# Performance work log

Measured on AMD Instinct MI355X. Metric: run time of the kernel, lower is better.

## Reference

```python
import jax, jax.numpy as jnp
import numpy as np

LSTM_SIZE = 512
MEM_SIZE = 2048
MEM_DIM = 256
NB_READS = 4
GAMMA = 0.95
EPS = 1e-8
B = 64
IN_RAW = 256
IN_TOTAL = IN_RAW + NB_READS * MEM_SIZE  # 8448
PARAM_DIM = (2 * MEM_DIM + 1) * NB_READS  # 2052


def setup_inputs() -> dict:
    key = jax.random.key(0)
    ks = jax.random.split(key, 8)
    s = 0.02
    return {
        "x": jax.random.normal(ks[0], (B, IN_RAW), jnp.float32),
        "M": jax.random.normal(ks[1], (B, MEM_SIZE, MEM_DIM), jnp.float32),
        "wu": jax.random.uniform(ks[2], (B, MEM_SIZE), jnp.float32),
        "wr": jax.random.uniform(ks[3], (B, NB_READS * MEM_SIZE), jnp.float32),
        "h0": jnp.zeros((LSTM_SIZE,), jnp.float32),
        "c0": jnp.zeros((LSTM_SIZE,), jnp.float32),
        "W_ih": jax.random.normal(ks[4], (4 * LSTM_SIZE, IN_TOTAL), jnp.float32) * s,
        "W_hh": jax.random.normal(ks[5], (4 * LSTM_SIZE, LSTM_SIZE), jnp.float32) * s,
        "b_ih": jnp.zeros((4 * LSTM_SIZE,), jnp.float32),
        "b_hh": jnp.zeros((4 * LSTM_SIZE,), jnp.float32),
        "W_p": jax.random.normal(ks[6], (PARAM_DIM, LSTM_SIZE), jnp.float32) * s,
        "b_p": jax.random.uniform(ks[7], (PARAM_DIM,), jnp.float32, -0.1, 0.1),
    }


def _lstm_scan(x_seq, h0, c0, W_ih, W_hh, b):
    # torch treats the 2-D input as an unbatched sequence of length B:
    # the recurrence runs across the batch axis with a single shared state.
    xW = x_seq @ W_ih.T + b  # [B, 4H] precomputed input contribution

    def step(carry, xw):
        h, c = carry
        g = xw + h @ W_hh.T
        i, f, gg, o = jnp.split(g, 4)
        c = jax.nn.sigmoid(f) * c + jax.nn.sigmoid(i) * jnp.tanh(gg)
        h = jax.nn.sigmoid(o) * jnp.tanh(c)
        return (h, c), h

    (hf, cf), hs = jax.lax.scan(step, (h0, c0), xW)
    return hs, hf, cf


def reference(x, M, wu, wr, h0, c0, W_ih, W_hh, b_ih, b_hh, W_p, b_p):
    ctrl_in = jnp.concatenate([x, wr], axis=-1)  # [B, IN_TOTAL]
    hs, hf, cf = _lstm_scan(ctrl_in, h0, c0, W_ih, W_hh, b_ih + b_hh)
    param = hs @ W_p.T + b_p  # [B, PARAM_DIM]

    nd = NB_READS * MEM_DIM
    k = jnp.tanh(param[:, :nd]).reshape(B, NB_READS, MEM_DIM)
    a = jnp.tanh(param[:, nd:2 * nd]).reshape(B, NB_READS, MEM_DIM)
    sig_alpha = jax.nn.sigmoid(param[:, -NB_READS:])  # [B, R]

    # least_used: topk(wu, k=MEM_SIZE) == full descending sort of indices
    order = jnp.argsort(-wu, axis=-1)  # [B, MEM_SIZE]
    lu_idx = order[:, -1]  # least used slot
    wlu = jax.nn.one_hot(order[:, -NB_READS:], MEM_SIZE, dtype=M.dtype).sum(1)  # [B, N]

    # read head addressing: cosine similarity softmax
    ip = jnp.einsum('brd,bnd->brn', k, M)  # [B, R, N]
    k_norm = jnp.sqrt(jnp.sum(k * k, -1))[:, :, None]
    M_norm = jnp.sqrt(jnp.sum(M * M, -1))[:, None, :]
    wr_t = jax.nn.softmax(ip / (k_norm * M_norm + EPS), axis=-1)  # [B, R, N]

    # write head addressing
    wr_prev3 = wr.reshape(B, NB_READS, MEM_SIZE)
    sa = sig_alpha[:, :, None]
    ww_t = sa * wr_prev3 + (1.0 - sa) * wlu[:, None, :]  # [B, R, N]

    wu_t = GAMMA * wu + wr_t.sum(1) + ww_t.sum(1)  # [B, N]

    erase = 1.0 - jax.nn.one_hot(lu_idx, MEM_SIZE, dtype=M.dtype)  # [B, N]
    M_t = M * erase[:, :, None] + jnp.einsum('brn,brd->bnd', ww_t, a)  # [B, N, D]
    r_t = jnp.einsum('brn,bnd->brd', wr_t, M_t).reshape(B, nd)  # [B, R*D]

    return jnp.concatenate([hs, r_t], axis=-1)  # [B, LSTM+R*D]
```

## Files before the change

### kernel.cpp

```cpp
#include <hip/hip_runtime.h>
#include <hip/hip_bf16.h>

#define BB 64
#define IN_RAW_ 256
#define KIN_ 8448
#define WRW 8192
#define PD_ 2052
#define XW_KS 11
#define XW_CH 768

__global__ __launch_bounds__(256) void k_xw_partial(
    const float* __restrict__ x, const float* __restrict__ wr,
    const float* __restrict__ Wih, float* __restrict__ xwp) {
  const int jb = blockIdx.x & 31;
  const int ks = blockIdx.x >> 5;
  const int j0 = jb << 6;
  const int k0 = ks * XW_CH;
  __shared__ __align__(16) float As[32][68];
  __shared__ __align__(16) float Bs[32][68];
  const int tid = threadIdx.x;
  const int ti = tid & 15, tj = tid >> 4;
  const int lt = tid >> 2, lq = tid & 3;
  float acc[4][4];
#pragma unroll
  for (int i = 0; i < 4; ++i)
#pragma unroll
    for (int j = 0; j < 4; ++j) acc[i][j] = 0.f;
  for (int kc = 0; kc < XW_CH; kc += 32) {
    __syncthreads();
    const int kb = k0 + kc + (lq << 3);
    float va[8], vb[8];
    if (kb < IN_RAW_) {
      const float* p = x + lt * IN_RAW_ + kb;
#pragma unroll
      for (int u = 0; u < 8; ++u) va[u] = p[u];
    } else {
      const float* p = wr + (size_t)lt * WRW + (kb - IN_RAW_);
#pragma unroll
      for (int u = 0; u < 8; ++u) va[u] = p[u];
    }
    {
      const float* p = Wih + (size_t)(j0 + lt) * KIN_ + kb;
#pragma unroll
      for (int u = 0; u < 8; ++u) vb[u] = p[u];
    }
#pragma unroll
    for (int u = 0; u < 8; ++u) As[(lq << 3) + u][lt] = va[u];
#pragma unroll
    for (int u = 0; u < 8; ++u) Bs[(lq << 3) + u][lt] = vb[u];
    __syncthreads();
#pragma unroll
    for (int kk = 0; kk < 32; ++kk) {
      const float4 a4 = *(const float4*)&As[kk][ti << 2];
      const float4 b4 = *(const float4*)&Bs[kk][tj << 2];
      const float av[4] = {a4.x, a4.y, a4.z, a4.w};
      const float bv[4] = {b4.x, b4.y, b4.z, b4.w};
#pragma unroll
      for (int i = 0; i < 4; ++i)
#pragma unroll
        for (int j = 0; j < 4; ++j) acc[i][j] = fmaf(av[i], bv[j], acc[i][j]);
    }
  }
#pragma unroll
  for (int i = 0; i < 4; ++i) {
    const int t = (ti << 2) + i;
    float* dst = xwp + ((size_t)(ks * BB + t) << 11) + j0 + (tj << 2);
    dst[0] = acc[i][0]; dst[1] = acc[i][1]; dst[2] = acc[i][2]; dst[3] = acc[i][3];
  }
}

__global__ __launch_bounds__(64, 1) void k_scan(
    const float* __restrict__ xwp, const float* __restrict__ bih,
    const float* __restrict__ bhh, const float* __restrict__ Whh,
    const float* __restrict__ h0, const float* __restrict__ c0,
    unsigned long long* __restrict__ ht, unsigned long long* __restrict__ xwt,
    float* __restrict__ out, const float* __restrict__ wu,
    int* __restrict__ t4) {
  const int W = blockIdx.x;
  const int l = threadIdx.x;
  if (W >= 192) {
    const int t = W - 192;
    for (int i = 0; i < 32; ++i) {
      const int col = (i << 6) + l;
      float s = bih[col] + bhh[col];
#pragma unroll
      for (int ks = 0; ks < XW_KS; ++ks)
        s += xwp[(size_t)ks * 131072 + (t << 11) + col];
      const unsigned long long pk =
          (1ull << 32) | (unsigned long long)__float_as_uint(s);
      __hip_atomic_store(xwt + (t << 11) + col, pk, __ATOMIC_RELAXED,
                         __HIP_MEMORY_SCOPE_AGENT);
    }
    return;
  }
  if (W >= 128) {
    const int b = W - 128;
    float val[32];
#pragma unroll
    for (int i = 0; i < 32; ++i) val[i] = wu[(b << 11) + (i << 6) + l];
    for (int pick = 0; pick < 4; ++pick) {
      float bv = 3.4e38f; int bi = -1;
#pragma unroll
      for (int i = 0; i < 32; ++i) {
        const int n = (i << 6) + l;
        const float v = val[i];
        if (v < bv || (v == bv && n > bi)) { bv = v; bi = n; }
      }
#pragma unroll
      for (int s = 1; s < 64; s <<= 1) {
        const float ov = __shfl_xor(bv, s);
        const int oi = __shfl_xor(bi, s);
        if (ov < bv || (ov == bv && oi > bi)) { bv = ov; bi = oi; }
      }
      if (l == 0) t4[(b << 2) + pick] = bi;
      if ((bi & 63) == l) val[bi >> 6] = 3.4e38f;
    }
    return;
  }
  const int d = l & 3;
  const int jj = (W << 2) + d;
  float wreg[16][8];
#pragma unroll
  for (int r = 0; r < 16; ++r) {
    const int row = ((r >> 2) << 9) + (W << 2) + (r & 3);
    const float* p = Whh + ((size_t)row << 9) + (l << 3);
#pragma unroll
    for (int u = 0; u < 8; ++u) wreg[r][u] = p[u];
  }
  float c = 0.f;
  if (l < 4) c = c0[jj];
  float h[8];
#pragma unroll
  for (int u = 0; u < 8; ++u) h[u] = h0[(l << 3) + u];

  for (int t = 0; t < 64; ++t) {
    float xv0 = 0, xv1 = 0, xv2 = 0, xv3 = 0;
    if (l < 4) {
      const unsigned long long* xp = xwt + (t << 11) + jj;
      unsigned long long x0, x1, x2, x3;
      for (;;) {
        x0 = __hip_atomic_load(xp, __ATOMIC_RELAXED, __HIP_MEMORY_SCOPE_AGENT);
        x1 = __hip_atomic_load(xp + 512, __ATOMIC_RELAXED, __HIP_MEMORY_SCOPE_AGENT);
        x2 = __hip_atomic_load(xp + 1024, __ATOMIC_RELAXED, __HIP_MEMORY_SCOPE_AGENT);
        x3 = __hip_atomic_load(xp + 1536, __ATOMIC_RELAXED, __HIP_MEMORY_SCOPE_AGENT);
        if ((unsigned)((x0 & x1 & x2 & x3) >> 32) == 1u) break;
      }
      xv0 = __uint_as_float((unsigned)x0);
      xv1 = __uint_as_float((unsigned)x1);
      xv2 = __uint_as_float((unsigned)x2);
      xv3 = __uint_as_float((unsigned)x3);
    }
    if (t > 0) {
      const unsigned long long* hp = ht + (t << 9) + (l << 3);
      unsigned long long va[8], vb[8];
#pragma unroll
      for (int u = 0; u < 8; ++u)
        va[u] = __hip_atomic_load(hp + u, __ATOMIC_RELAXED, __HIP_MEMORY_SCOPE_AGENT);
      for (;;) {
#pragma unroll
        for (int u = 0; u < 8; ++u)
          vb[u] = __hip_atomic_load(hp + u, __ATOMIC_RELAXED, __HIP_MEMORY_SCOPE_AGENT);
        bool ra = true;
#pragma unroll
        for (int u = 0; u < 8; ++u) ra &= ((unsigned)(va[u] >> 32) == (unsigned)t);
        if (ra) break;
#pragma unroll
        for (int u = 0; u < 8; ++u)
          va[u] = __hip_atomic_load(hp + u, __ATOMIC_RELAXED, __HIP_MEMORY_SCOPE_AGENT);
        bool rb_ = true;
#pragma unroll
        for (int u = 0; u < 8; ++u) rb_ &= ((unsigned)(vb[u] >> 32) == (unsigned)t);
        if (rb_) {
#pragma unroll
          for (int u = 0; u < 8; ++u) va[u] = vb[u];
          break;
        }
      }
#pragma unroll
      for (int u = 0; u < 8; ++u) h[u] = __uint_as_float((unsigned)va[u]);
    }
    float pr[16];
#pragma unroll
    for (int r = 0; r < 16; ++r) {
      float s = 0.f;
#pragma unroll
      for (int u = 0; u < 8; ++u) s = fmaf(wreg[r][u], h[u], s);
      pr[r] = s;
    }
    float v8[8], v4[4], v2[2], v1;
    {
      const bool b0 = (l & 1) != 0;
#pragma unroll
      for (int j = 0; j < 8; ++j) {
        const float keep = b0 ? pr[2 * j + 1] : pr[2 * j];
        const float send = b0 ? pr[2 * j] : pr[2 * j + 1];
        v8[j] = keep + __shfl_xor(send, 1);
      }
    }
    {
      const bool b1 = (l & 2) != 0;
#pragma unroll
      for (int j = 0; j < 4; ++j) {
        const float keep = b1 ? v8[2 * j + 1] : v8[2 * j];
        const float send = b1 ? v8[2 * j] : v8[2 * j + 1];
        v4[j] = keep + __shfl_xor(send, 2);
      }
    }
    {
      const bool b2 = (l & 4) != 0;
#pragma unroll
      for (int j = 0; j < 2; ++j) {
        const float keep = b2 ? v4[2 * j + 1] : v4[2 * j];
        const float send = b2 ? v4[2 * j] : v4[2 * j + 1];
        v2[j] = keep + __shfl_xor(send, 4);
      }
    }
    {
      const bool b3 = (l & 8) != 0;
      const float keep = b3 ? v2[1] : v2[0];
      const float send = b3 ? v2[0] : v2[1];
      v1 = keep + __shfl_xor(send, 8);
    }
    v1 += __shfl_xor(v1, 16);
    v1 += __shfl_xor(v1, 32);
    const float gi_ = __shfl(v1, d);
    const float gf_ = __shfl(v1, d + 4);
    const float gg_ = __shfl(v1, d + 8);
    const float go_ = __shfl(v1, d + 12);
    if (l < 4) {
      const float gi = gi_ + xv0;
      const float gf = gf_ + xv1;
      const float gg = gg_ + xv2;
      const float go = go_ + xv3;
      const float si = 1.f / (1.f + __expf(-gi));
      const float sf = 1.f / (1.f + __expf(-gf));
      const float so = 1.f / (1.f + __expf(-go));
      const float tg = 2.f / (1.f + __expf(-2.f * gg)) - 1.f;
      c = sf * c + si * tg;
      const float tc = 2.f / (1.f + __expf(-2.f * c)) - 1.f;
      const float hnew = so * tc;
      const unsigned long long pk =
          ((unsigned long long)(unsigned)(t + 1) << 32) |
          (unsigned long long)__float_as_uint(hnew);
      __hip_atomic_store(ht + ((t + 1) << 9) + jj, pk, __ATOMIC_RELAXED,
                         __HIP_MEMORY_SCOPE_AGENT);
      out[t * 1536 + jj] = hnew;
    }
  }
}

__global__ __launch_bounds__(256) void k_param(
    const float* __restrict__ outbuf, const float* __restrict__ Wp,
    const float* __restrict__ bp, float* __restrict__ km,
    float* __restrict__ am, float* __restrict__ sa) {
  const int j0 = blockIdx.x << 6;
  __shared__ __align__(16) float As[32][68];
  __shared__ __align__(16) float Bs[32][68];
  const int tid = threadIdx.x;
  const int ti = tid & 15, tj = tid >> 4;
  const int lt = tid >> 2, lq = tid & 3;
  float acc[4][4];
#pragma unroll
  for (int i = 0; i < 4; ++i)
#pragma unroll
    for (int j = 0; j < 4; ++j) acc[i][j] = 0.f;
  for (int kc = 0; kc < 512; kc += 32) {
    __syncthreads();
    const int kb = kc + (lq << 3);
    float va[8], vb[8];
    {
      const float* p = outbuf + lt * 1536 + kb;
#pragma unroll
      for (int u = 0; u < 8; ++u) va[u] = p[u];
    }
    const int brow = j0 + lt;
    if (brow < PD_) {
      const float* p = Wp + (size_t)brow * 512 + kb;
#pragma unroll
      for (int u = 0; u < 8; ++u) vb[u] = p[u];
    } else {
#pragma unroll
      for (int u = 0; u < 8; ++u) vb[u] = 0.f;
    }
#pragma unroll
    for (int u = 0; u < 8; ++u) As[(lq << 3) + u][lt] = va[u];
#pragma unroll
    for (int u = 0; u < 8; ++u) Bs[(lq << 3) + u][lt] = vb[u];
    __syncthreads();
#pragma unroll
    for (int kk = 0; kk < 32; ++kk) {
      const float4 a4 = *(const float4*)&As[kk][ti << 2];
      const float4 b4 = *(const float4*)&Bs[kk][tj << 2];
      const float av[4] = {a4.x, a4.y, a4.z, a4.w};
      const float bv[4] = {b4.x, b4.y, b4.z, b4.w};
#pragma unroll
      for (int i = 0; i < 4; ++i)
#pragma unroll
        for (int j = 0; j < 4; ++j) acc[i][j] = fmaf(av[i], bv[j], acc[i][j]);
    }
  }
#pragma unroll
  for (int i = 0; i < 4; ++i) {
    const int b = (ti << 2) + i;
#pragma unroll
    for (int j = 0; j < 4; ++j) {
      const int col = j0 + (tj << 2) + j;
      if (col < PD_) {
        const float v = acc[i][j] + bp[col];
        if (col < 1024) km[(b << 10) + col] = tanhf(v);
        else if (col < 2048) am[(b << 10) + col - 1024] = tanhf(v);
        else sa[(b << 2) + col - 2048] = 1.f / (1.f + expf(-v));
      }
    }
  }
}

__global__ __launch_bounds__(256) void k_ipv(
    const float* __restrict__ M, const float* __restrict__ km,
    const float* __restrict__ wr_in, const int* __restrict__ t4,
    float* __restrict__ pacc, float* __restrict__ pscal) {
  const int b = blockIdx.x >> 3;
  const int sl = blockIdx.x & 7;
  const int tid = threadIdx.x;
  const int wv = tid >> 6, l = tid & 63;
  const int g = l >> 4, j = l & 15;
  __shared__ float kns[4];
  __shared__ float t4eL[4][4];
  __shared__ __align__(16) float accW[4][4][256];
  __shared__ float SdW[4][4][4];
  __shared__ float ssW[4][4];
  if (tid < 16) t4eL[tid >> 2][tid & 3] = 0.f;
  {
    const float* kp = km + (((b << 2) + wv) << 8);
    float sq = 0.f;
#pragma unroll
    for (int i = 0; i < 4; ++i) { const float v = kp[l + (i << 6)]; sq = fmaf(v, v, sq); }
    sq += __shfl_xor(sq, 1);  sq += __shfl_xor(sq, 2);  sq += __shfl_xor(sq, 4);
    sq += __shfl_xor(sq, 8);  sq += __shfl_xor(sq, 16); sq += __shfl_xor(sq, 32);
    if (l == 0) kns[wv] = sqrtf(sq);
  }
  float kr[4][16];
#pragma unroll
  for (int r = 0; r < 4; ++r)
#pragma unroll
    for (int cc = 0; cc < 4; ++cc) {
      const float4 kv = *(const float4*)(km + (((b << 2) + r) << 8) + (cc << 6) + (j << 2));
      kr[r][(cc << 2) + 0] = kv.x; kr[r][(cc << 2) + 1] = kv.y;
      kr[r][(cc << 2) + 2] = kv.z; kr[r][(cc << 2) + 3] = kv.w;
    }
  int t4v[4];
#pragma unroll
  for (int ii = 0; ii < 4; ++ii) t4v[ii] = t4[(b << 2) + ii];
  __syncthreads();
  const float kn0 = kns[0], kn1 = kns[1], kn2 = kns[2], kn3 = kns[3];
  float aacc[4][16];
#pragma unroll
  for (int r = 0; r < 4; ++r)
#pragma unroll
    for (int k = 0; k < 16; ++k) aacc[r][k] = 0.f;
  float ssum[4] = {0.f, 0.f, 0.f, 0.f};
  float sdp[4] = {0.f, 0.f, 0.f, 0.f};
  for (int it = 0; it < 16; ++it) {
    const int n = (sl << 8) + (wv << 6) + (it << 2) + g;
    const float* mrow = M + (((size_t)b << 11) + n) * 256;
    float4 m4[4];
#pragma unroll
    for (int cc = 0; cc < 4; ++cc)
      m4[cc] = *(const float4*)(mrow + (cc << 6) + (j << 2));
    float s0 = 0.f, s1 = 0.f, s2 = 0.f, s3 = 0.f, sm = 0.f;
#pragma unroll
    for (int cc = 0; cc < 4; ++cc) {
      const float mv[4] = {m4[cc].x, m4[cc].y, m4[cc].z, m4[cc].w};
#pragma unroll
      for (int e = 0; e < 4; ++e) {
        sm = fmaf(mv[e], mv[e], sm);
        s0 = fmaf(kr[0][(cc << 2) + e], mv[e], s0);
        s1 = fmaf(kr[1][(cc << 2) + e], mv[e], s1);
        s2 = fmaf(kr[2][(cc << 2) + e], mv[e], s2);
        s3 = fmaf(kr[3][(cc << 2) + e], mv[e], s3);
      }
    }
    s0 += __shfl_xor(s0, 1); s0 += __shfl_xor(s0, 2); s0 += __shfl_xor(s0, 4); s0 += __shfl_xor(s0, 8);
    s1 += __shfl_xor(s1, 1); s1 += __shfl_xor(s1, 2); s1 += __shfl_xor(s1, 4); s1 += __shfl_xor(s1, 8);
    s2 += __shfl_xor(s2, 1); s2 += __shfl_xor(s2, 2); s2 += __shfl_xor(s2, 4); s2 += __shfl_xor(s2, 8);
    s3 += __shfl_xor(s3, 1); s3 += __shfl_xor(s3, 2); s3 += __shfl_xor(s3, 4); s3 += __shfl_xor(s3, 8);
    sm += __shfl_xor(sm, 1); sm += __shfl_xor(sm, 2); sm += __shfl_xor(sm, 4); sm += __shfl_xor(sm, 8);
    const float mnv = sqrtf(sm);
    float ev[4];
    ev[0] = __expf(s0 / fmaf(kn0, mnv, 1e-8f));
    ev[1] = __expf(s1 / fmaf(kn1, mnv, 1e-8f));
    ev[2] = __expf(s2 / fmaf(kn2, mnv, 1e-8f));
    ev[3] = __expf(s3 / fmaf(kn3, mnv, 1e-8f));
#pragma unroll
    for (int r = 0; r < 4; ++r) {
      ssum[r] += ev[r];
#pragma unroll
      for (int cc = 0; cc < 4; ++cc) {
        aacc[r][(cc << 2) + 0] = fmaf(ev[r], m4[cc].x, aacc[r][(cc << 2) + 0]);
        aacc[r][(cc << 2) + 1] = fmaf(ev[r], m4[cc].y, aacc[r][(cc << 2) + 1]);
        aacc[r][(cc << 2) + 2] = fmaf(ev[r], m4[cc].z, aacc[r][(cc << 2) + 2]);
        aacc[r][(cc << 2) + 3] = fmaf(ev[r], m4[cc].w, aacc[r][(cc << 2) + 3]);
      }
    }
    if (j < 4) {
      const float wq = wr_in[((size_t)b << 13) + (j << 11) + n];
#pragma unroll
      for (int r = 0; r < 4; ++r) sdp[r] = fmaf(ev[r], wq, sdp[r]);
    }
#pragma unroll
    for (int ii = 0; ii < 4; ++ii)
      if (n == t4v[ii] && j == 0) {
#pragma unroll
        for (int r = 0; r < 4; ++r) t4eL[ii][r] = ev[r];
      }
  }
#pragma unroll
  for (int r = 0; r < 4; ++r) {
    float v = ssum[r];
    v += __shfl_xor(v, 1);  v += __shfl_xor(v, 2);  v += __shfl_xor(v, 4);
    v += __shfl_xor(v, 8);  v += __shfl_xor(v, 16); v += __shfl_xor(v, 32);
    if (l == 0) ssW[wv][r] = v * 0.0625f;
    float sdv = sdp[r];
    sdv += __shfl_xor(sdv, 16);
    sdv += __shfl_xor(sdv, 32);
    if (l < 4) SdW[wv][l][r] = sdv;
  }
#pragma unroll
  for (int r = 0; r < 4; ++r)
#pragma unroll
    for (int k = 0; k < 16; ++k) {
      float v = aacc[r][k];
      v += __shfl_xor(v, 16);
      v += __shfl_xor(v, 32);
      aacc[r][k] = v;
    }
  if (l < 16) {
#pragma unroll
    for (int r = 0; r < 4; ++r)
#pragma unroll
      for (int cc = 0; cc < 4; ++cc)
#pragma unroll
        for (int ee = 0; ee < 4; ++ee)
          accW[wv][r][(cc << 6) + (l << 2) + ee] = aacc[r][(cc << 2) + ee];
  }
  __syncthreads();
  const int slice = (b << 3) + sl;
#pragma unroll
  for (int i = 0; i < 4; ++i) {
    const int e = tid + (i << 8);
    const float s4 = accW[0][i][tid] + accW[1][i][tid] + accW[2][i][tid] + accW[3][i][tid];
    pacc[((size_t)slice << 10) + e] = s4;
  }
  if (tid < 4)
    pscal[(slice << 6) + tid] = ssW[0][tid] + ssW[1][tid] + ssW[2][tid] + ssW[3][tid];
  if (tid < 16) {
    const int r = tid >> 2, q = tid & 3;
    pscal[(slice << 6) + 4 + (r << 2) + q] =
        SdW[0][q][r] + SdW[1][q][r] + SdW[2][q][r] + SdW[3][q][r];
    pscal[(slice << 6) + 20 + tid] = t4eL[tid >> 2][tid & 3];
  }
}

__global__ __launch_bounds__(256) void k_fin(
    const float* __restrict__ pacc, const float* __restrict__ pscal,
    const float* __restrict__ sa_g, const float* __restrict__ am,
    const float* __restrict__ M, const int* __restrict__ t4,
    float* __restrict__ out) {
  const int b = blockIdx.x;
  const int tid = threadIdx.x;
  __shared__ float Zs[4], Sl[16], wlu4[4], teL[4][4];
  if (tid < 4) {
    float z = 0.f;
    for (int sl = 0; sl < 8; ++sl) z += pscal[(((b << 3) + sl) << 6) + tid];
    Zs[tid] = z;
  }
  if (tid >= 16 && tid < 32) {
    const int ii = (tid - 16) >> 2, r = (tid - 16) & 3;
    float te = 0.f;
    for (int sl = 0; sl < 8; ++sl)
      te += pscal[(((b << 3) + sl) << 6) + 20 + (ii << 2) + r];
    teL[ii][r] = te;
  }
  __syncthreads();
  if (tid < 16) {
    const int r = tid >> 2, q = tid & 3;
    float sd = 0.f;
    for (int sl = 0; sl < 8; ++sl)
      sd += pscal[(((b << 3) + sl) << 6) + 4 + (r << 2) + q];
    const float Z = Zs[r];
    const float t4s = (teL[0][r] + teL[1][r] + teL[2][r] + teL[3][r]) / Z;
    const float sv = sa_g[(b << 2) + q];
    Sl[(r << 2) + q] = sv * (sd / Z) + (1.f - sv) * t4s;
    if (q == 0) wlu4[r] = teL[0][r] / Z;
  }
  __syncthreads();
  const int luv = t4[b << 2];
#pragma unroll
  for (int i = 0; i < 4; ++i) {
    const int e = tid + (i << 8);
    float s = 0.f;
    for (int sl = 0; sl < 8; ++sl)
      s += pacc[((size_t)(((b << 3) + sl)) << 10) + e];
    s /= Zs[i];
    s -= wlu4[i] * M[(((size_t)b << 11) + luv) * 256 + tid];
#pragma unroll
    for (int q = 0; q < 4; ++q)
      s = fmaf(Sl[(i << 2) + q], am[(((b << 2) + q) << 8) + tid], s);
    out[b * 1536 + 512 + e] = s;
  }
}

extern "C" void kernel_launch(void* const* d_in, const int* in_sizes, int n_in,
                              void* d_out, int out_size, void* d_ws, size_t ws_size,
                              hipStream_t stream) {
  (void)in_sizes; (void)n_in; (void)out_size;
  const float* x   = (const float*)d_in[0];
  const float* M   = (const float*)d_in[1];
  const float* wu  = (const float*)d_in[2];
  const float* wr  = (const float*)d_in[3];
  const float* h0  = (const float*)d_in[4];
  const float* c0  = (const float*)d_in[5];
  const float* Wih = (const float*)d_in[6];
  const float* Whh = (const float*)d_in[7];
  const float* bih = (const float*)d_in[8];
  const float* bhh = (const float*)d_in[9];
  const float* Wp  = (const float*)d_in[10];
  const float* bp  = (const float*)d_in[11];
  float* out = (float*)d_out;
  char* ws = (char*)d_ws;
  if (ws_size < 9836544u) return;

  float* xwp  = (float*)(ws + 0);
  float* km   = (float*)(ws + 5767168);
  float* am   = (float*)(ws + 6029312);
  float* sa   = (float*)(ws + 6291456);
  int*   t4   = (int*)(ws + 6292480);
  float* pacc = (float*)(ws + 6293504);
  float* pscal= (float*)(ws + 8390656);
  unsigned long long* ht  = (unsigned long long*)(ws + 8521728);
  unsigned long long* xwt = (unsigned long long*)(ws + 8787968);

  (void)hipMemsetAsync(ws + 8521728, 0, 266240 + 1048576, stream);
  hipLaunchKernelGGL(k_xw_partial, dim3(352), dim3(256), 0, stream, x, wr, Wih, xwp);
  hipLaunchKernelGGL(k_scan, dim3(256), dim3(64), 0, stream,
                     xwp, bih, bhh, Whh, h0, c0, ht, xwt, out, wu, t4);
  hipLaunchKernelGGL(k_param, dim3(33), dim3(256), 0, stream, out, Wp, bp, km, am, sa);
  hipLaunchKernelGGL(k_ipv, dim3(512), dim3(256), 0, stream, M, km, wr, t4, pacc, pscal);
  hipLaunchKernelGGL(k_fin, dim3(64), dim3(256), 0, stream,
                     pacc, pscal, sa, am, M, t4, out);
}
```

Baseline: 250.3 us.

## Widen input-projection GEMM tile to 128 columns and resplit K into sixteen

Each block of the input-projection GEMM now computes 64x128 outputs, with a 4x8 register tile per thread, instead of 64x64. The K dimension is split into 16 chunks of 544 (the last is 288), which gives exactly 256 blocks. The aim is to halve redundant loads of the activation tile, use wider vector stores, and fill the GPU in a single wave instead of 1.4 waves. In exchange there are more register accumulators and more partial-sum slices (16 instead of 11), which the scan kernel must read and reduce, and the workspace grows to hold them.

After: 256.7 us. 1.03x slower.

```diff
diff --git a/kernel.cpp b/kernel.cpp
--- a/kernel.cpp
+++ b/kernel.cpp
@@ -6,30 +6,30 @@
 #define KIN_ 8448
 #define WRW 8192
 #define PD_ 2052
-#define XW_KS 11
-#define XW_CH 768
+#define XW_KS 16
 
 __global__ __launch_bounds__(256) void k_xw_partial(
     const float* __restrict__ x, const float* __restrict__ wr,
     const float* __restrict__ Wih, float* __restrict__ xwp) {
-  const int jb = blockIdx.x & 31;
-  const int ks = blockIdx.x >> 5;
-  const int j0 = jb << 6;
-  const int k0 = ks * XW_CH;
+  const int cb = blockIdx.x & 15;
+  const int ks = blockIdx.x >> 4;
+  const int j0 = cb << 7;
+  const int k0 = ks * 544;
+  const int klen = (ks == 15) ? 288 : 544;
   __shared__ __align__(16) float As[32][68];
-  __shared__ __align__(16) float Bs[32][68];
+  __shared__ __align__(16) float Bs[32][136];
   const int tid = threadIdx.x;
   const int ti = tid & 15, tj = tid >> 4;
   const int lt = tid >> 2, lq = tid & 3;
-  float acc[4][4];
+  float acc[4][8];
 #pragma unroll
   for (int i = 0; i < 4; ++i)
 #pragma unroll
-    for (int j = 0; j < 4; ++j) acc[i][j] = 0.f;
-  for (int kc = 0; kc < XW_CH; kc += 32) {
+    for (int j = 0; j < 8; ++j) acc[i][j] = 0.f;
+  for (int kc = 0; kc < klen; kc += 32) {
     __syncthreads();
     const int kb = k0 + kc + (lq << 3);
-    float va[8], vb[8];
+    float va[8], vb0[8], vb1[8];
     if (kb < IN_RAW_) {
       const float* p = x + lt * IN_RAW_ + kb;
 #pragma unroll
@@ -42,30 +42,38 @@
     {
       const float* p = Wih + (size_t)(j0 + lt) * KIN_ + kb;
 #pragma unroll
-      for (int u = 0; u < 8; ++u) vb[u] = p[u];
+      for (int u = 0; u < 8; ++u) vb0[u] = p[u];
+      const float* p2 = Wih + (size_t)(j0 + 64 + lt) * KIN_ + kb;
+#pragma unroll
+      for (int u = 0; u < 8; ++u) vb1[u] = p2[u];
     }
 #pragma unroll
     for (int u = 0; u < 8; ++u) As[(lq << 3) + u][lt] = va[u];
 #pragma unroll
-    for (int u = 0; u < 8; ++u) Bs[(lq << 3) + u][lt] = vb[u];
+    for (int u = 0; u < 8; ++u) Bs[(lq << 3) + u][lt] = vb0[u];
+#pragma unroll
+    for (int u = 0; u < 8; ++u) Bs[(lq << 3) + u][64 + lt] = vb1[u];
     __syncthreads();
 #pragma unroll
     for (int kk = 0; kk < 32; ++kk) {
       const float4 a4 = *(const float4*)&As[kk][ti << 2];
-      const float4 b4 = *(const float4*)&Bs[kk][tj << 2];
+      const float4 b4a = *(const float4*)&Bs[kk][tj << 3];
+      const float4 b4b = *(const float4*)&Bs[kk][(tj << 3) + 4];
       const float av[4] = {a4.x, a4.y, a4.z, a4.w};
-      const float bv[4] = {b4.x, b4.y, b4.z, b4.w};
+      const float bv[8] = {b4a.x, b4a.y, b4a.z, b4a.w,
+                           b4b.x, b4b.y, b4b.z, b4b.w};
 #pragma unroll
       for (int i = 0; i < 4; ++i)
 #pragma unroll
-        for (int j = 0; j < 4; ++j) acc[i][j] = fmaf(av[i], bv[j], acc[i][j]);
+        for (int j = 0; j < 8; ++j) acc[i][j] = fmaf(av[i], bv[j], acc[i][j]);
     }
   }
 #pragma unroll
   for (int i = 0; i < 4; ++i) {
     const int t = (ti << 2) + i;
-    float* dst = xwp + ((size_t)(ks * BB + t) << 11) + j0 + (tj << 2);
-    dst[0] = acc[i][0]; dst[1] = acc[i][1]; dst[2] = acc[i][2]; dst[3] = acc[i][3];
+    float* dst = xwp + (size_t)ks * 131072 + (t << 11) + j0 + (tj << 3);
+    *(float4*)(dst) = make_float4(acc[i][0], acc[i][1], acc[i][2], acc[i][3]);
+    *(float4*)(dst + 4) = make_float4(acc[i][4], acc[i][5], acc[i][6], acc[i][7]);
   }
 }
 
@@ -528,20 +536,20 @@
   const float* bp  = (const float*)d_in[11];
   float* out = (float*)d_out;
   char* ws = (char*)d_ws;
-  if (ws_size < 9836544u) return;
+  if (ws_size < 12457984u) return;
 
   float* xwp  = (float*)(ws + 0);
-  float* km   = (float*)(ws + 5767168);
-  float* am   = (float*)(ws + 6029312);
-  float* sa   = (float*)(ws + 6291456);
-  int*   t4   = (int*)(ws + 6292480);
-  float* pacc = (float*)(ws + 6293504);
-  float* pscal= (float*)(ws + 8390656);
-  unsigned long long* ht  = (unsigned long long*)(ws + 8521728);
-  unsigned long long* xwt = (unsigned long long*)(ws + 8787968);
-
-  (void)hipMemsetAsync(ws + 8521728, 0, 266240 + 1048576, stream);
-  hipLaunchKernelGGL(k_xw_partial, dim3(352), dim3(256), 0, stream, x, wr, Wih, xwp);
+  float* km   = (float*)(ws + 8388608);
+  float* am   = (float*)(ws + 8650752);
+  float* sa   = (float*)(ws + 8912896);
+  int*   t4   = (int*)(ws + 8913920);
+  float* pacc = (float*)(ws + 8914944);
+  float* pscal= (float*)(ws + 11012096);
+  unsigned long long* ht  = (unsigned long long*)(ws + 11143168);
+  unsigned long long* xwt = (unsigned long long*)(ws + 11409408);
+
+  (void)hipMemsetAsync(ws + 11143168, 0, 266240 + 1048576, stream);
+  hipLaunchKernelGGL(k_xw_partial, dim3(256), dim3(256), 0, stream, x, wr, Wih, xwp);
   hipLaunchKernelGGL(k_scan, dim3(256), dim3(64), 0, stream,
                      xwp, bih, bhh, Whh, h0, c0, ht, xwt, out, wu, t4);
   hipLaunchKernelGGL(k_param, dim3(33), dim3(256), 0, stream, out, Wp, bp, km, am, sa);
```
